# Kernel optimization log

Hardware: AMD Instinct MI355X
Metric: run time of the kernel (lower is better)

The kernel has to match this reference:

```python
import jax, jax.numpy as jnp
import numpy as np

B, K, N, D, H, DOUT = 16, 8, 196, 768, 3072, 768


def setup_inputs() -> dict:
    key = jax.random.key(0)
    ks = jax.random.split(key, 5)
    scale_w1 = 1.0 / np.sqrt(D)
    scale_w2 = 1.0 / np.sqrt(H)
    return {
        "slots": jax.random.normal(ks[0], (B, K, D), dtype=jnp.float32),
        "pos_embed": jax.random.normal(ks[1], (N, D), dtype=jnp.float32) * 0.02,
        "map_alpha": jax.random.normal(ks[2], (N, DOUT), dtype=jnp.float32) * 0.02,
        "W1": jax.random.normal(ks[3], (D, H), dtype=jnp.float32) * scale_w1,
        "b1": jnp.zeros((H,), dtype=jnp.float32),
        "W2": jax.random.normal(ks[4], (H, DOUT), dtype=jnp.float32) * scale_w2,
        "b2": jnp.zeros((DOUT,), dtype=jnp.float32),
    }


def reference(slots, pos_embed, map_alpha, W1, b1, W2, b2):
    b, k, d = slots.shape
    n = pos_embed.shape[0]
    # broadcast slots over patches and add positional embedding: (B,K,N,D)
    tokens = slots[:, :, None, :] + pos_embed[None, None, :, :]
    # 2-layer MLP with ReLU
    h = jax.nn.relu(jnp.einsum('bknd,dh->bknh', tokens, W1) + b1)
    y_k = jnp.einsum('bknh,ho->bkno', h, W2) + b2  # (B,K,N,DOUT)
    # softmax over K of map_alpha expanded over (B,K); identical across K -> uniform 1/K,
    # computed explicitly for faithfulness to the original module
    m_k = jax.nn.softmax(jnp.broadcast_to(map_alpha[None, None, :, :], (b, k, n, map_alpha.shape[1])), axis=1)
    y = jnp.einsum('bknd,bknd->bnd', y_k, m_k)
    return y
```

## Files before the change

### kernel.cpp

```cpp
#include <hip/hip_runtime.h>
#include <hip/hip_bf16.h>
#include <stdint.h>


typedef __attribute__((ext_vector_type(8))) short bf16x8;
typedef __attribute__((ext_vector_type(4))) float f32x4;

#define AS1 __attribute__((address_space(1)))
#define AS3 __attribute__((address_space(3)))

#define WAIT_VM(N) asm volatile("s_waitcnt vmcnt(" #N ")" ::: "memory")
#define BAR()      asm volatile("s_barrier" ::: "memory")
#define BAR_LDS()  asm volatile("s_waitcnt lgkmcnt(0)\ns_barrier" ::: "memory")

static __device__ __forceinline__ void gld_lds16(const void* g, void* l) {
    __builtin_amdgcn_global_load_lds((const AS1 unsigned int*)g,
                                     (AS3 unsigned int*)l, 16, 0, 0);
}

static __device__ __forceinline__ unsigned short f2bf(float f) {
    union { float f; unsigned int u; } v; v.f = f;
    unsigned int u = v.u;
    return (unsigned short)((u + 0x7fffu + ((u >> 16) & 1u)) >> 16);
}

__global__ void k_prep(const float* __restrict__ W1, unsigned short* __restrict__ W1t,
                       const float* __restrict__ S, const float* __restrict__ P,
                       unsigned short* __restrict__ A1) {
    int idx = blockIdx.x * blockDim.x + threadIdx.x;
    const int C1n = 96 * 3072;
    const int PKn = 96 * 384;
    if (idx < C1n) {
        int r  = idx % 3072;
        int kc = idx / 3072;
        unsigned int po[4];
        #pragma unroll
        for (int j = 0; j < 4; ++j) {
            unsigned short lo = f2bf(W1[(size_t)(kc * 8 + 2 * j) * 3072 + r]);
            unsigned short hi = f2bf(W1[(size_t)(kc * 8 + 2 * j + 1) * 3072 + r]);
            po[j] = (unsigned int)lo | ((unsigned int)hi << 16);
        }
        size_t dst = ((size_t)(r >> 6) * 12 + (kc >> 3)) * 4096
                   + (size_t)((kc & 7) * 64 + (r & 63)) * 8;
        *(uint4*)(W1t + dst) = make_uint4(po[0], po[1], po[2], po[3]);
    } else if (idx < C1n + PKn) {
        int t = idx - C1n;
        int r  = t % 384;
        int kc = t / 384;
        uint4 o = make_uint4(0u, 0u, 0u, 0u);
        if (r < 324) {
            const float* src = (r < 128) ? (S + (size_t)r * 768 + kc * 8)
                                         : (P + (size_t)(r - 128) * 768 + kc * 8);
            float4 a = *(const float4*)(src);
            float4 b = *(const float4*)(src + 4);
            o.x = (unsigned int)f2bf(a.x) | ((unsigned int)f2bf(a.y) << 16);
            o.y = (unsigned int)f2bf(a.z) | ((unsigned int)f2bf(a.w) << 16);
            o.z = (unsigned int)f2bf(b.x) | ((unsigned int)f2bf(b.y) << 16);
            o.w = (unsigned int)f2bf(b.z) | ((unsigned int)f2bf(b.w) << 16);
        }
        size_t dst = ((size_t)(r >> 6) * 12 + (kc >> 3)) * 4096
                   + (size_t)((kc & 7) * 64 + (r & 63)) * 8;
        *(uint4*)(A1 + dst) = o;
    }
}

__global__ void k_hbar_w2t(const float* __restrict__ C1, const float* __restrict__ b1,
                           unsigned short* __restrict__ Hb,
                           const float* __restrict__ W2, unsigned short* __restrict__ W2t) {
    const int bid = blockIdx.x;
    const int tid = threadIdx.x;
    if (bid >= 4800) {
        int idx = (bid - 4800) * 256 + tid;
        int r  = idx % 768;
        int kc = idx / 768;
        unsigned int po[4];
        #pragma unroll
        for (int j = 0; j < 4; ++j) {
            unsigned short lo = f2bf(W2[(size_t)(kc * 8 + 2 * j) * 768 + r]);
            unsigned short hi = f2bf(W2[(size_t)(kc * 8 + 2 * j + 1) * 768 + r]);
            po[j] = (unsigned int)lo | ((unsigned int)hi << 16);
        }
        size_t dst = ((size_t)(r >> 6) * 48 + (kc >> 3)) * 4096
                   + (size_t)((kc & 7) * 64 + (r & 63)) * 8;
        *(uint4*)(W2t + dst) = make_uint4(po[0], po[1], po[2], po[3]);
        return;
    }
    const int bx   = bid % 50;
    const int yq   = bid / 50;
    const int lane = tid & 63;
    const int wv   = tid >> 6;
    const int hc   = yq * 4 + wv;
    const int h0   = hc * 8;
    int bn = bx * 64 + lane;
    if (bn > 3135) bn = 3135;
    const int b = bn / 196;
    const int n = bn - b * 196;
    const float* prow = C1 + (size_t)(128 + n) * 3072 + h0;
    float4 pA = *(const float4*)(prow);
    float4 pB = *(const float4*)(prow + 4);
    float4 bA = *(const float4*)(b1 + h0);
    float4 bB = *(const float4*)(b1 + h0 + 4);
    float pb[8] = { pA.x + bA.x, pA.y + bA.y, pA.z + bA.z, pA.w + bA.w,
                    pB.x + bB.x, pB.y + bB.y, pB.z + bB.z, pB.w + bB.w };
    float acc[8] = {};
    #pragma unroll
    for (int k = 0; k < 8; ++k) {
        const float* srow = C1 + (size_t)(b * 8 + k) * 3072 + h0;
        float4 sA_ = *(const float4*)(srow);
        float4 sB_ = *(const float4*)(srow + 4);
        acc[0] += fmaxf(sA_.x + pb[0], 0.f);
        acc[1] += fmaxf(sA_.y + pb[1], 0.f);
        acc[2] += fmaxf(sA_.z + pb[2], 0.f);
        acc[3] += fmaxf(sA_.w + pb[3], 0.f);
        acc[4] += fmaxf(sB_.x + pb[4], 0.f);
        acc[5] += fmaxf(sB_.y + pb[5], 0.f);
        acc[6] += fmaxf(sB_.z + pb[6], 0.f);
        acc[7] += fmaxf(sB_.w + pb[7], 0.f);
    }
    unsigned int w0 = (unsigned int)f2bf(acc[0] * 0.125f) | ((unsigned int)f2bf(acc[1] * 0.125f) << 16);
    unsigned int w1 = (unsigned int)f2bf(acc[2] * 0.125f) | ((unsigned int)f2bf(acc[3] * 0.125f) << 16);
    unsigned int w2 = (unsigned int)f2bf(acc[4] * 0.125f) | ((unsigned int)f2bf(acc[5] * 0.125f) << 16);
    unsigned int w3 = (unsigned int)f2bf(acc[6] * 0.125f) | ((unsigned int)f2bf(acc[7] * 0.125f) << 16);
    size_t dst = ((size_t)bx * 48 + (hc >> 3)) * 4096
               + (size_t)((hc & 7) * 64 + lane) * 8;
    *(uint4*)(Hb + dst) = make_uint4(w0, w1, w2, w3);
}

__launch_bounds__(256)
__global__ void gemm_tiled(const unsigned short* __restrict__ A,
                           const unsigned short* __restrict__ Bt,
                           float* __restrict__ C,
                           int Mstore, int Nd, int KT) {
    __shared__ unsigned short sm[3 * 8192];

    const int tid  = threadIdx.x;
    const int lane = tid & 63;
    const int wave = tid >> 6;
    const int wm = wave >> 1, wn = wave & 1;
    const int q = lane >> 4, l16 = lane & 15;

    const int id = blockIdx.x;
    const int j  = id >> 3;
    const int nt = (id & 7) * 6 + j % 6;
    const int rt = j / 6;

    const unsigned short* Ab = A  + (size_t)rt * KT * 4096;
    const unsigned short* Bb = Bt + (size_t)nt * KT * 4096;

    f32x4 acc[2][2] = {};
    const int offA = (wm * 32 + l16) * 8;
    const int offB = 4096 + (wn * 32 + l16) * 8;

    auto stage = [&](int i, unsigned short* d) {
        const unsigned short* Ag = Ab + (size_t)i * 4096;
        const unsigned short* Bg = Bb + (size_t)i * 4096;
        gld_lds16(Ag + tid * 8,        d + tid * 8);
        gld_lds16(Ag + 2048 + tid * 8, d + 2048 + tid * 8);
        gld_lds16(Bg + tid * 8,        d + 4096 + tid * 8);
        gld_lds16(Bg + 2048 + tid * 8, d + 6144 + tid * 8);
    };
    auto compute = [&](const unsigned short* buf) {
        #pragma unroll
        for (int ks = 0; ks < 2; ++ks) {
            const int ko = (ks * 4 + q) * 512;
            bf16x8 af0 = *(const bf16x8*)(buf + ko + offA);
            bf16x8 af1 = *(const bf16x8*)(buf + ko + offA + 128);
            bf16x8 bf0 = *(const bf16x8*)(buf + ko + offB);
            bf16x8 bf1 = *(const bf16x8*)(buf + ko + offB + 128);
            acc[0][0] = __builtin_amdgcn_mfma_f32_16x16x32_bf16(af0, bf0, acc[0][0], 0, 0, 0);
            acc[0][1] = __builtin_amdgcn_mfma_f32_16x16x32_bf16(af0, bf1, acc[0][1], 0, 0, 0);
            acc[1][0] = __builtin_amdgcn_mfma_f32_16x16x32_bf16(af1, bf0, acc[1][0], 0, 0, 0);
            acc[1][1] = __builtin_amdgcn_mfma_f32_16x16x32_bf16(af1, bf1, acc[1][1], 0, 0, 0);
        }
    };

    unsigned short* s0 = sm;
    unsigned short* s1 = sm + 8192;
    unsigned short* s2 = sm + 16384;

    stage(0, s0);
    stage(1, s1);
    for (int i = 0; i < KT; i += 3) {
        stage(i + 2, s2); WAIT_VM(8);
        BAR(); compute(s0); BAR_LDS();
        if (i + 3 < KT) { stage(i + 3, s0); WAIT_VM(8); } else { WAIT_VM(4); }
        BAR(); compute(s1); BAR_LDS();
        if (i + 4 < KT) { stage(i + 4, s1); WAIT_VM(8); }
        else if (i + 3 < KT) { WAIT_VM(4); }
        else { WAIT_VM(0); }
        BAR(); compute(s2);
        if (i + 3 < KT) BAR_LDS();
    }

    const int row0 = rt * 64 + wm * 32;
    const int col0 = nt * 64 + wn * 32;
    #pragma unroll
    for (int ii = 0; ii < 2; ++ii) {
        #pragma unroll
        for (int jj = 0; jj < 2; ++jj) {
            int col = col0 + jj * 16 + l16;
            #pragma unroll
            for (int r = 0; r < 4; ++r) {
                int row = row0 + ii * 16 + q * 4 + r;
                if (row < Mstore) C[(size_t)row * Nd + col] = acc[ii][jj][r];
            }
        }
    }
}

__launch_bounds__(512)
__global__ void k_gemm2(const unsigned short* __restrict__ Hb,
                        const unsigned short* __restrict__ W2t,
                        const float* __restrict__ b2, float* __restrict__ out) {
    __shared__ unsigned short sm[3 * 12288];

    const int tid  = threadIdx.x;
    const int lane = tid & 63;
    const int wave = tid >> 6;
    const int wm = wave >> 1, wn = wave & 1;
    const int q = lane >> 4, l16 = lane & 15;

    const int id = blockIdx.x;
    int rt, nt;
    if (id < 288) { rt = (id / 96) * 8 + (id & 7); nt = (id % 96) >> 3; }
    else          { rt = 24; nt = id - 288; }

    const unsigned short* A0b = Hb  + ((size_t)(2 * rt)     * 48) * 4096;
    const unsigned short* A1b = Hb  + ((size_t)(2 * rt + 1) * 48) * 4096;
    const unsigned short* Bb  = W2t + ((size_t)nt * 48) * 4096;

    f32x4 acc[2][2] = {};

    auto stage = [&](int i, unsigned short* d) {
        gld_lds16(A0b + (size_t)i * 4096 + tid * 8, d + tid * 8);
        gld_lds16(A1b + (size_t)i * 4096 + tid * 8, d + 4096 + tid * 8);
        gld_lds16(Bb  + (size_t)i * 4096 + tid * 8, d + 8192 + tid * 8);
    };

    const int r0 = wm * 32 + l16;
    const int aoff0 = (r0 >> 6) * 4096 + (r0 & 63) * 8;
    const int r1 = wm * 32 + 16 + l16;
    const int aoff1 = (r1 >> 6) * 4096 + (r1 & 63) * 8;
    const int boff  = 8192 + (wn * 32 + l16) * 8;

    auto compute = [&](const unsigned short* buf) {
        #pragma unroll
        for (int ks = 0; ks < 2; ++ks) {
            const int ko = (ks * 4 + q) * 512;
            bf16x8 af0 = *(const bf16x8*)(buf + aoff0 + ko);
            bf16x8 af1 = *(const bf16x8*)(buf + aoff1 + ko);
            bf16x8 bf0 = *(const bf16x8*)(buf + boff + ko);
            bf16x8 bf1 = *(const bf16x8*)(buf + boff + ko + 128);
            acc[0][0] = __builtin_amdgcn_mfma_f32_16x16x32_bf16(af0, bf0, acc[0][0], 0, 0, 0);
            acc[0][1] = __builtin_amdgcn_mfma_f32_16x16x32_bf16(af0, bf1, acc[0][1], 0, 0, 0);
            acc[1][0] = __builtin_amdgcn_mfma_f32_16x16x32_bf16(af1, bf0, acc[1][0], 0, 0, 0);
            acc[1][1] = __builtin_amdgcn_mfma_f32_16x16x32_bf16(af1, bf1, acc[1][1], 0, 0, 0);
        }
    };

    unsigned short* s0 = sm;
    unsigned short* s1 = sm + 12288;
    unsigned short* s2 = sm + 24576;

    stage(0, s0);
    stage(1, s1);
    for (int i = 0; i < 48; i += 3) {
        stage(i + 2, s2); WAIT_VM(6);
        BAR(); compute(s0); BAR_LDS();
        if (i + 3 < 48) { stage(i + 3, s0); WAIT_VM(6); } else { WAIT_VM(3); }
        BAR(); compute(s1); BAR_LDS();
        if (i + 4 < 48) { stage(i + 4, s1); WAIT_VM(6); }
        else if (i + 3 < 48) { WAIT_VM(3); }
        else { WAIT_VM(0); }
        BAR(); compute(s2);
        if (i + 3 < 48) BAR_LDS();
    }

    const int row0 = rt * 128 + wm * 32;
    const int col0 = nt * 64 + wn * 32;
    #pragma unroll
    for (int ii = 0; ii < 2; ++ii) {
        #pragma unroll
        for (int jj = 0; jj < 2; ++jj) {
            int col = col0 + jj * 16 + l16;
            float bv = b2[col];
            #pragma unroll
            for (int r = 0; r < 4; ++r) {
                int row = row0 + ii * 16 + q * 4 + r;
                if (row < 3136) out[(size_t)row * 768 + col] = acc[ii][jj][r] + bv;
            }
        }
    }
}

extern "C" void kernel_launch(void* const* d_in, const int* in_sizes, int n_in,
                              void* d_out, int out_size, void* d_ws, size_t ws_size,
                              hipStream_t stream) {
    const float* slots  = (const float*)d_in[0];
    const float* pos    = (const float*)d_in[1];
    const float* W1     = (const float*)d_in[3];
    const float* b1     = (const float*)d_in[4];
    const float* W2     = (const float*)d_in[5];
    const float* b2     = (const float*)d_in[6];
    float* out = (float*)d_out;

    size_t off = 0;
    auto alloc = [&](size_t bytes) {
        void* p = (char*)d_ws + off;
        off += (bytes + 255) & ~(size_t)255;
        return p;
    };
    unsigned short* W1t = (unsigned short*)alloc((size_t)3072 * 768 * 2);
    unsigned short* W2t = (unsigned short*)alloc((size_t)768 * 3072 * 2);
    unsigned short* A1  = (unsigned short*)alloc((size_t)384 * 768 * 2);
    float*          C1  = (float*)alloc((size_t)384 * 3072 * 4);
    unsigned short* Hb  = (unsigned short*)alloc((size_t)50 * 48 * 4096 * 2);

    k_prep<<<1296, 256, 0, stream>>>(W1, W1t, slots, pos, A1);
    gemm_tiled<<<288, 256, 0, stream>>>(A1, W1t, C1, 324, 3072, 12);
    k_hbar_w2t<<<5952, 256, 0, stream>>>(C1, b1, Hb, W2, W2t);
    k_gemm2<<<300, 512, 0, stream>>>(Hb, W2t, b2, out);
}
```

Before: 129.9 us.

## Fuse four kernels into one persistent kernel with software grid barriers

Replaces the four separate launches (prep, GEMM1, hbar/W2 transpose, GEMM2) with a single persistent 384-block kernel whose phases are separated by atomic-counter grid barriers. W2 conversion moves into the first prep phase. GEMM1 is retiled to 64x128 tiles with 512 threads, and both GEMMs switch from triple to double buffering. The aim is to remove launch gaps and tail effects, at the cost of spin-wait barriers, fewer blocks for the GEMM phases, and reliance on all 384 blocks being co-resident. The barrier reset scheme via a MAGIC flag in workspace could be fragile across repeated calls.

```diff
diff --git a/kernel.cpp b/kernel.cpp
--- a/kernel.cpp
+++ b/kernel.cpp
@@ -12,6 +12,9 @@
 #define WAIT_VM(N) asm volatile("s_waitcnt vmcnt(" #N ")" ::: "memory")
 #define BAR()      asm volatile("s_barrier" ::: "memory")
 #define BAR_LDS()  asm volatile("s_waitcnt lgkmcnt(0)\ns_barrier" ::: "memory")
+
+#define NB 384u
+#define MAGIC 0x13572468u
 
 static __device__ __forceinline__ void gld_lds16(const void* g, void* l) {
     __builtin_amdgcn_global_load_lds((const AS1 unsigned int*)g,
@@ -24,270 +27,254 @@
     return (unsigned short)((u + 0x7fffu + ((u >> 16) & 1u)) >> 16);
 }
 
-__global__ void k_prep(const float* __restrict__ W1, unsigned short* __restrict__ W1t,
-                       const float* __restrict__ S, const float* __restrict__ P,
-                       unsigned short* __restrict__ A1) {
-    int idx = blockIdx.x * blockDim.x + threadIdx.x;
-    const int C1n = 96 * 3072;
-    const int PKn = 96 * 384;
-    if (idx < C1n) {
-        int r  = idx % 3072;
-        int kc = idx / 3072;
-        unsigned int po[4];
-        #pragma unroll
-        for (int j = 0; j < 4; ++j) {
-            unsigned short lo = f2bf(W1[(size_t)(kc * 8 + 2 * j) * 3072 + r]);
-            unsigned short hi = f2bf(W1[(size_t)(kc * 8 + 2 * j + 1) * 3072 + r]);
-            po[j] = (unsigned int)lo | ((unsigned int)hi << 16);
-        }
-        size_t dst = ((size_t)(r >> 6) * 12 + (kc >> 3)) * 4096
-                   + (size_t)((kc & 7) * 64 + (r & 63)) * 8;
-        *(uint4*)(W1t + dst) = make_uint4(po[0], po[1], po[2], po[3]);
-    } else if (idx < C1n + PKn) {
-        int t = idx - C1n;
-        int r  = t % 384;
-        int kc = t / 384;
-        uint4 o = make_uint4(0u, 0u, 0u, 0u);
-        if (r < 324) {
-            const float* src = (r < 128) ? (S + (size_t)r * 768 + kc * 8)
-                                         : (P + (size_t)(r - 128) * 768 + kc * 8);
-            float4 a = *(const float4*)(src);
-            float4 b = *(const float4*)(src + 4);
-            o.x = (unsigned int)f2bf(a.x) | ((unsigned int)f2bf(a.y) << 16);
-            o.y = (unsigned int)f2bf(a.z) | ((unsigned int)f2bf(a.w) << 16);
-            o.z = (unsigned int)f2bf(b.x) | ((unsigned int)f2bf(b.y) << 16);
-            o.w = (unsigned int)f2bf(b.z) | ((unsigned int)f2bf(b.w) << 16);
-        }
-        size_t dst = ((size_t)(r >> 6) * 12 + (kc >> 3)) * 4096
-                   + (size_t)((kc & 7) * 64 + (r & 63)) * 8;
-        *(uint4*)(A1 + dst) = o;
-    }
-}
-
-__global__ void k_hbar_w2t(const float* __restrict__ C1, const float* __restrict__ b1,
-                           unsigned short* __restrict__ Hb,
-                           const float* __restrict__ W2, unsigned short* __restrict__ W2t) {
-    const int bid = blockIdx.x;
-    const int tid = threadIdx.x;
-    if (bid >= 4800) {
-        int idx = (bid - 4800) * 256 + tid;
-        int r  = idx % 768;
-        int kc = idx / 768;
-        unsigned int po[4];
-        #pragma unroll
-        for (int j = 0; j < 4; ++j) {
-            unsigned short lo = f2bf(W2[(size_t)(kc * 8 + 2 * j) * 768 + r]);
-            unsigned short hi = f2bf(W2[(size_t)(kc * 8 + 2 * j + 1) * 768 + r]);
-            po[j] = (unsigned int)lo | ((unsigned int)hi << 16);
-        }
-        size_t dst = ((size_t)(r >> 6) * 48 + (kc >> 3)) * 4096
-                   + (size_t)((kc & 7) * 64 + (r & 63)) * 8;
-        *(uint4*)(W2t + dst) = make_uint4(po[0], po[1], po[2], po[3]);
-        return;
-    }
-    const int bx   = bid % 50;
-    const int yq   = bid / 50;
-    const int lane = tid & 63;
-    const int wv   = tid >> 6;
-    const int hc   = yq * 4 + wv;
-    const int h0   = hc * 8;
-    int bn = bx * 64 + lane;
-    if (bn > 3135) bn = 3135;
-    const int b = bn / 196;
-    const int n = bn - b * 196;
-    const float* prow = C1 + (size_t)(128 + n) * 3072 + h0;
-    float4 pA = *(const float4*)(prow);
-    float4 pB = *(const float4*)(prow + 4);
-    float4 bA = *(const float4*)(b1 + h0);
-    float4 bB = *(const float4*)(b1 + h0 + 4);
-    float pb[8] = { pA.x + bA.x, pA.y + bA.y, pA.z + bA.z, pA.w + bA.w,
-                    pB.x + bB.x, pB.y + bB.y, pB.z + bB.z, pB.w + bB.w };
-    float acc[8] = {};
-    #pragma unroll
-    for (int k = 0; k < 8; ++k) {
-        const float* srow = C1 + (size_t)(b * 8 + k) * 3072 + h0;
-        float4 sA_ = *(const float4*)(srow);
-        float4 sB_ = *(const float4*)(srow + 4);
-        acc[0] += fmaxf(sA_.x + pb[0], 0.f);
-        acc[1] += fmaxf(sA_.y + pb[1], 0.f);
-        acc[2] += fmaxf(sA_.z + pb[2], 0.f);
-        acc[3] += fmaxf(sA_.w + pb[3], 0.f);
-        acc[4] += fmaxf(sB_.x + pb[4], 0.f);
-        acc[5] += fmaxf(sB_.y + pb[5], 0.f);
-        acc[6] += fmaxf(sB_.z + pb[6], 0.f);
-        acc[7] += fmaxf(sB_.w + pb[7], 0.f);
-    }
-    unsigned int w0 = (unsigned int)f2bf(acc[0] * 0.125f) | ((unsigned int)f2bf(acc[1] * 0.125f) << 16);
-    unsigned int w1 = (unsigned int)f2bf(acc[2] * 0.125f) | ((unsigned int)f2bf(acc[3] * 0.125f) << 16);
-    unsigned int w2 = (unsigned int)f2bf(acc[4] * 0.125f) | ((unsigned int)f2bf(acc[5] * 0.125f) << 16);
-    unsigned int w3 = (unsigned int)f2bf(acc[6] * 0.125f) | ((unsigned int)f2bf(acc[7] * 0.125f) << 16);
-    size_t dst = ((size_t)bx * 48 + (hc >> 3)) * 4096
-               + (size_t)((hc & 7) * 64 + lane) * 8;
-    *(uint4*)(Hb + dst) = make_uint4(w0, w1, w2, w3);
-}
-
-__launch_bounds__(256)
-__global__ void gemm_tiled(const unsigned short* __restrict__ A,
-                           const unsigned short* __restrict__ Bt,
-                           float* __restrict__ C,
-                           int Mstore, int Nd, int KT) {
-    __shared__ unsigned short sm[3 * 8192];
-
+static __device__ __forceinline__ void grid_barrier(unsigned* slot) {
+    __syncthreads();
+    if (threadIdx.x == 0) {
+        __threadfence();
+        __hip_atomic_fetch_add(slot, 1u, __ATOMIC_ACQ_REL, __HIP_MEMORY_SCOPE_AGENT);
+        while (__hip_atomic_load(slot, __ATOMIC_RELAXED, __HIP_MEMORY_SCOPE_AGENT) < NB)
+            __builtin_amdgcn_s_sleep(16);
+        __threadfence();
+    }
+    __syncthreads();
+}
+
+__launch_bounds__(512, 4)
+__global__ void k_fused(const float* __restrict__ slots, const float* __restrict__ pos,
+                        const float* __restrict__ W1, const float* __restrict__ b1,
+                        const float* __restrict__ W2, const float* __restrict__ b2,
+                        unsigned* __restrict__ bar,
+                        unsigned short* __restrict__ W1t, unsigned short* __restrict__ W2t,
+                        unsigned short* __restrict__ A1, float* __restrict__ C1,
+                        unsigned short* __restrict__ Hb, float* __restrict__ out) {
+    __shared__ unsigned short sm[2 * 12288];
     const int tid  = threadIdx.x;
     const int lane = tid & 63;
     const int wave = tid >> 6;
-    const int wm = wave >> 1, wn = wave & 1;
-    const int q = lane >> 4, l16 = lane & 15;
-
-    const int id = blockIdx.x;
-    const int j  = id >> 3;
-    const int nt = (id & 7) * 6 + j % 6;
-    const int rt = j / 6;
-
-    const unsigned short* Ab = A  + (size_t)rt * KT * 4096;
-    const unsigned short* Bb = Bt + (size_t)nt * KT * 4096;
-
-    f32x4 acc[2][2] = {};
-    const int offA = (wm * 32 + l16) * 8;
-    const int offB = 4096 + (wn * 32 + l16) * 8;
-
-    auto stage = [&](int i, unsigned short* d) {
-        const unsigned short* Ag = Ab + (size_t)i * 4096;
-        const unsigned short* Bg = Bb + (size_t)i * 4096;
-        gld_lds16(Ag + tid * 8,        d + tid * 8);
-        gld_lds16(Ag + 2048 + tid * 8, d + 2048 + tid * 8);
-        gld_lds16(Bg + tid * 8,        d + 4096 + tid * 8);
-        gld_lds16(Bg + 2048 + tid * 8, d + 6144 + tid * 8);
-    };
-    auto compute = [&](const unsigned short* buf) {
+    const int q    = lane >> 4;
+    const int l16  = lane & 15;
+
+    if (blockIdx.x == 0 && tid == 0) {
+        __hip_atomic_store(&bar[1], 0u, __ATOMIC_RELAXED, __HIP_MEMORY_SCOPE_AGENT);
+        __hip_atomic_store(&bar[2], 0u, __ATOMIC_RELAXED, __HIP_MEMORY_SCOPE_AGENT);
+        __hip_atomic_store(&bar[3], 0u, __ATOMIC_RELAXED, __HIP_MEMORY_SCOPE_AGENT);
+        __hip_atomic_store(&bar[0], MAGIC, __ATOMIC_RELEASE, __HIP_MEMORY_SCOPE_AGENT);
+    }
+
+    for (int idx = blockIdx.x * 512 + tid; idx < 626688; idx += NB * 512) {
+        if (idx < 294912) {
+            int r  = idx % 3072;
+            int kc = idx / 3072;
+            unsigned int po[4];
+            #pragma unroll
+            for (int j = 0; j < 4; ++j) {
+                unsigned short lo = f2bf(W1[(size_t)(kc * 8 + 2 * j) * 3072 + r]);
+                unsigned short hi = f2bf(W1[(size_t)(kc * 8 + 2 * j + 1) * 3072 + r]);
+                po[j] = (unsigned int)lo | ((unsigned int)hi << 16);
+            }
+            size_t dst = ((size_t)(r >> 6) * 12 + (kc >> 3)) * 4096
+                       + (size_t)((kc & 7) * 64 + (r & 63)) * 8;
+            *(uint4*)(W1t + dst) = make_uint4(po[0], po[1], po[2], po[3]);
+        } else if (idx < 331776) {
+            int t = idx - 294912;
+            int r  = t % 384;
+            int kc = t / 384;
+            uint4 o = make_uint4(0u, 0u, 0u, 0u);
+            if (r < 324) {
+                const float* src = (r < 128) ? (slots + (size_t)r * 768 + kc * 8)
+                                             : (pos + (size_t)(r - 128) * 768 + kc * 8);
+                float4 a = *(const float4*)(src);
+                float4 b = *(const float4*)(src + 4);
+                o.x = (unsigned int)f2bf(a.x) | ((unsigned int)f2bf(a.y) << 16);
+                o.y = (unsigned int)f2bf(a.z) | ((unsigned int)f2bf(a.w) << 16);
+                o.z = (unsigned int)f2bf(b.x) | ((unsigned int)f2bf(b.y) << 16);
+                o.w = (unsigned int)f2bf(b.z) | ((unsigned int)f2bf(b.w) << 16);
+            }
+            size_t dst = ((size_t)(r >> 6) * 12 + (kc >> 3)) * 4096
+                       + (size_t)((kc & 7) * 64 + (r & 63)) * 8;
+            *(uint4*)(A1 + dst) = o;
+        } else {
+            int t = idx - 331776;
+            int r  = t % 768;
+            int kc = t / 768;
+            unsigned int po[4];
+            #pragma unroll
+            for (int j = 0; j < 4; ++j) {
+                unsigned short lo = f2bf(W2[(size_t)(kc * 8 + 2 * j) * 768 + r]);
+                unsigned short hi = f2bf(W2[(size_t)(kc * 8 + 2 * j + 1) * 768 + r]);
+                po[j] = (unsigned int)lo | ((unsigned int)hi << 16);
+            }
+            size_t dst = ((size_t)(r >> 6) * 48 + (kc >> 3)) * 4096
+                       + (size_t)((kc & 7) * 64 + (r & 63)) * 8;
+            *(uint4*)(W2t + dst) = make_uint4(po[0], po[1], po[2], po[3]);
+        }
+    }
+    __syncthreads();
+    if (tid == 0) {
+        while (__hip_atomic_load(&bar[0], __ATOMIC_RELAXED, __HIP_MEMORY_SCOPE_AGENT) != MAGIC)
+            __builtin_amdgcn_s_sleep(16);
+        __threadfence();
+        __hip_atomic_fetch_add(&bar[1], 1u, __ATOMIC_ACQ_REL, __HIP_MEMORY_SCOPE_AGENT);
+        while (__hip_atomic_load(&bar[1], __ATOMIC_RELAXED, __HIP_MEMORY_SCOPE_AGENT) < NB)
+            __builtin_amdgcn_s_sleep(16);
+        __threadfence();
+    }
+    __syncthreads();
+
+    if (blockIdx.x < 144) {
+        const int rt = blockIdx.x / 24;
+        const int nt = blockIdx.x % 24;
+        const unsigned short* Ab = A1  + (size_t)rt * 12 * 4096;
+        const unsigned short* B0 = W1t + (size_t)(2 * nt)     * 12 * 4096;
+        const unsigned short* B1 = W1t + (size_t)(2 * nt + 1) * 12 * 4096;
+        const int wm = wave >> 2;
+        const int wn = wave & 3;
+        f32x4 acc[2][2] = {};
+        auto stage = [&](int i, unsigned short* d) {
+            gld_lds16(Ab + (size_t)i * 4096 + tid * 8, d + tid * 8);
+            gld_lds16(B0 + (size_t)i * 4096 + tid * 8, d + 4096 + tid * 8);
+            gld_lds16(B1 + (size_t)i * 4096 + tid * 8, d + 8192 + tid * 8);
+        };
+        const int aoff = (wm * 32 + l16) * 8;
+        const int boff = 4096 + (wn >> 1) * 4096 + ((wn & 1) * 32 + l16) * 8;
+        auto compute = [&](const unsigned short* buf) {
+            #pragma unroll
+            for (int ks = 0; ks < 2; ++ks) {
+                const int ko = (ks * 4 + q) * 512;
+                bf16x8 af0 = *(const bf16x8*)(buf + ko + aoff);
+                bf16x8 af1 = *(const bf16x8*)(buf + ko + aoff + 128);
+                bf16x8 bf0 = *(const bf16x8*)(buf + ko + boff);
+                bf16x8 bf1 = *(const bf16x8*)(buf + ko + boff + 128);
+                acc[0][0] = __builtin_amdgcn_mfma_f32_16x16x32_bf16(af0, bf0, acc[0][0], 0, 0, 0);
+                acc[0][1] = __builtin_amdgcn_mfma_f32_16x16x32_bf16(af0, bf1, acc[0][1], 0, 0, 0);
+                acc[1][0] = __builtin_amdgcn_mfma_f32_16x16x32_bf16(af1, bf0, acc[1][0], 0, 0, 0);
+                acc[1][1] = __builtin_amdgcn_mfma_f32_16x16x32_bf16(af1, bf1, acc[1][1], 0, 0, 0);
+            }
+        };
+        stage(0, sm);
+        #pragma unroll 1
+        for (int i = 0; i < 12; ++i) {
+            unsigned short* cur = sm + (i & 1) * 12288;
+            unsigned short* nxt = sm + ((i + 1) & 1) * 12288;
+            if (i + 1 < 12) { stage(i + 1, nxt); WAIT_VM(3); } else { WAIT_VM(0); }
+            BAR();
+            compute(cur);
+            if (i + 1 < 12) BAR_LDS();
+        }
+        const int row0 = rt * 64 + wm * 32;
+        const int col0 = nt * 128 + ((wn >> 1) * 64) + (wn & 1) * 32;
         #pragma unroll
-        for (int ks = 0; ks < 2; ++ks) {
-            const int ko = (ks * 4 + q) * 512;
-            bf16x8 af0 = *(const bf16x8*)(buf + ko + offA);
-            bf16x8 af1 = *(const bf16x8*)(buf + ko + offA + 128);
-            bf16x8 bf0 = *(const bf16x8*)(buf + ko + offB);
-            bf16x8 bf1 = *(const bf16x8*)(buf + ko + offB + 128);
-            acc[0][0] = __builtin_amdgcn_mfma_f32_16x16x32_bf16(af0, bf0, acc[0][0], 0, 0, 0);
-            acc[0][1] = __builtin_amdgcn_mfma_f32_16x16x32_bf16(af0, bf1, acc[0][1], 0, 0, 0);
-            acc[1][0] = __builtin_amdgcn_mfma_f32_16x16x32_bf16(af1, bf0, acc[1][0], 0, 0, 0);
-            acc[1][1] = __builtin_amdgcn_mfma_f32_16x16x32_bf16(af1, bf1, acc[1][1], 0, 0, 0);
-        }
-    };
-
-    unsigned short* s0 = sm;
-    unsigned short* s1 = sm + 8192;
-    unsigned short* s2 = sm + 16384;
-
-    stage(0, s0);
-    stage(1, s1);
-    for (int i = 0; i < KT; i += 3) {
-        stage(i + 2, s2); WAIT_VM(8);
-        BAR(); compute(s0); BAR_LDS();
-        if (i + 3 < KT) { stage(i + 3, s0); WAIT_VM(8); } else { WAIT_VM(4); }
-        BAR(); compute(s1); BAR_LDS();
-        if (i + 4 < KT) { stage(i + 4, s1); WAIT_VM(8); }
-        else if (i + 3 < KT) { WAIT_VM(4); }
-        else { WAIT_VM(0); }
-        BAR(); compute(s2);
-        if (i + 3 < KT) BAR_LDS();
-    }
-
-    const int row0 = rt * 64 + wm * 32;
-    const int col0 = nt * 64 + wn * 32;
-    #pragma unroll
-    for (int ii = 0; ii < 2; ++ii) {
+        for (int ii = 0; ii < 2; ++ii) {
+            #pragma unroll
+            for (int jj = 0; jj < 2; ++jj) {
+                int col = col0 + jj * 16 + l16;
+                #pragma unroll
+                for (int r = 0; r < 4; ++r) {
+                    int row = row0 + ii * 16 + q * 4 + r;
+                    if (row < 324) C1[(size_t)row * 3072 + col] = acc[ii][jj][r];
+                }
+            }
+        }
+    }
+    grid_barrier(&bar[2]);
+
+    for (int u = blockIdx.x; u < 2400; u += NB) {
+        const int bx = u / 48;
+        const int hg = u - bx * 48;
+        const int hc = hg * 8 + wave;
+        const int h0 = hc * 8;
+        int bn = bx * 64 + lane;
+        if (bn > 3135) bn = 3135;
+        const int b = bn / 196;
+        const int n = bn - b * 196;
+        const float* prow = C1 + (size_t)(128 + n) * 3072 + h0;
+        float4 pA = *(const float4*)(prow);
+        float4 pB = *(const float4*)(prow + 4);
+        float4 bA = *(const float4*)(b1 + h0);
+        float4 bB = *(const float4*)(b1 + h0 + 4);
+        float pb[8] = { pA.x + bA.x, pA.y + bA.y, pA.z + bA.z, pA.w + bA.w,
+                        pB.x + bB.x, pB.y + bB.y, pB.z + bB.z, pB.w + bB.w };
+        float acc[8] = {};
         #pragma unroll
-        for (int jj = 0; jj < 2; ++jj) {
-            int col = col0 + jj * 16 + l16;
-            #pragma unroll
-            for (int r = 0; r < 4; ++r) {
-                int row = row0 + ii * 16 + q * 4 + r;
-                if (row < Mstore) C[(size_t)row * Nd + col] = acc[ii][jj][r];
-            }
-        }
-    }
-}
-
-__launch_bounds__(512)
-__global__ void k_gemm2(const unsigned short* __restrict__ Hb,
-                        const unsigned short* __restrict__ W2t,
-                        const float* __restrict__ b2, float* __restrict__ out) {
-    __shared__ unsigned short sm[3 * 12288];
-
-    const int tid  = threadIdx.x;
-    const int lane = tid & 63;
-    const int wave = tid >> 6;
-    const int wm = wave >> 1, wn = wave & 1;
-    const int q = lane >> 4, l16 = lane & 15;
-
-    const int id = blockIdx.x;
-    int rt, nt;
-    if (id < 288) { rt = (id / 96) * 8 + (id & 7); nt = (id % 96) >> 3; }
-    else          { rt = 24; nt = id - 288; }
-
-    const unsigned short* A0b = Hb  + ((size_t)(2 * rt)     * 48) * 4096;
-    const unsigned short* A1b = Hb  + ((size_t)(2 * rt + 1) * 48) * 4096;
-    const unsigned short* Bb  = W2t + ((size_t)nt * 48) * 4096;
-
-    f32x4 acc[2][2] = {};
-
-    auto stage = [&](int i, unsigned short* d) {
-        gld_lds16(A0b + (size_t)i * 4096 + tid * 8, d + tid * 8);
-        gld_lds16(A1b + (size_t)i * 4096 + tid * 8, d + 4096 + tid * 8);
-        gld_lds16(Bb  + (size_t)i * 4096 + tid * 8, d + 8192 + tid * 8);
-    };
-
-    const int r0 = wm * 32 + l16;
-    const int aoff0 = (r0 >> 6) * 4096 + (r0 & 63) * 8;
-    const int r1 = wm * 32 + 16 + l16;
-    const int aoff1 = (r1 >> 6) * 4096 + (r1 & 63) * 8;
-    const int boff  = 8192 + (wn * 32 + l16) * 8;
-
-    auto compute = [&](const unsigned short* buf) {
+        for (int k = 0; k < 8; ++k) {
+            const float* srow = C1 + (size_t)(b * 8 + k) * 3072 + h0;
+            float4 sA_ = *(const float4*)(srow);
+            float4 sB_ = *(const float4*)(srow + 4);
+            acc[0] += fmaxf(sA_.x + pb[0], 0.f);
+            acc[1] += fmaxf(sA_.y + pb[1], 0.f);
+            acc[2] += fmaxf(sA_.z + pb[2], 0.f);
+            acc[3] += fmaxf(sA_.w + pb[3], 0.f);
+            acc[4] += fmaxf(sB_.x + pb[4], 0.f);
+            acc[5] += fmaxf(sB_.y + pb[5], 0.f);
+            acc[6] += fmaxf(sB_.z + pb[6], 0.f);
+            acc[7] += fmaxf(sB_.w + pb[7], 0.f);
+        }
+        unsigned int w0 = (unsigned int)f2bf(acc[0] * 0.125f) | ((unsigned int)f2bf(acc[1] * 0.125f) << 16);
+        unsigned int w1 = (unsigned int)f2bf(acc[2] * 0.125f) | ((unsigned int)f2bf(acc[3] * 0.125f) << 16);
+        unsigned int w2 = (unsigned int)f2bf(acc[4] * 0.125f) | ((unsigned int)f2bf(acc[5] * 0.125f) << 16);
+        unsigned int w3 = (unsigned int)f2bf(acc[6] * 0.125f) | ((unsigned int)f2bf(acc[7] * 0.125f) << 16);
+        size_t dst = ((size_t)bx * 48 + hg) * 4096 + (size_t)(wave * 64 + lane) * 8;
+        *(uint4*)(Hb + dst) = make_uint4(w0, w1, w2, w3);
+    }
+    grid_barrier(&bar[3]);
+
+    if (blockIdx.x < 300) {
+        const int id = blockIdx.x;
+        int rt, nt;
+        if (id < 288) { rt = (id / 96) * 8 + (id & 7); nt = (id % 96) >> 3; }
+        else          { rt = 24; nt = id - 288; }
+        const unsigned short* A0b = Hb  + ((size_t)(2 * rt)     * 48) * 4096;
+        const unsigned short* A1b = Hb  + ((size_t)(2 * rt + 1) * 48) * 4096;
+        const unsigned short* Bb  = W2t + ((size_t)nt * 48) * 4096;
+        const int wm = wave >> 1, wn = wave & 1;
+        f32x4 acc[2][2] = {};
+        auto stage = [&](int i, unsigned short* d) {
+            gld_lds16(A0b + (size_t)i * 4096 + tid * 8, d + tid * 8);
+            gld_lds16(A1b + (size_t)i * 4096 + tid * 8, d + 4096 + tid * 8);
+            gld_lds16(Bb  + (size_t)i * 4096 + tid * 8, d + 8192 + tid * 8);
+        };
+        const int r0 = wm * 32 + l16;
+        const int aoff0 = (r0 >> 6) * 4096 + (r0 & 63) * 8;
+        const int r1 = wm * 32 + 16 + l16;
+        const int aoff1 = (r1 >> 6) * 4096 + (r1 & 63) * 8;
+        const int boff  = 8192 + (wn * 32 + l16) * 8;
+        auto compute = [&](const unsigned short* buf) {
+            #pragma unroll
+            for (int ks = 0; ks < 2; ++ks) {
+                const int ko = (ks * 4 + q) * 512;
+                bf16x8 af0 = *(const bf16x8*)(buf + aoff0 + ko);
+                bf16x8 af1 = *(const bf16x8*)(buf + aoff1 + ko);
+                bf16x8 bf0 = *(const bf16x8*)(buf + boff + ko);
+                bf16x8 bf1 = *(const bf16x8*)(buf + boff + ko + 128);
+                acc[0][0] = __builtin_amdgcn_mfma_f32_16x16x32_bf16(af0, bf0, acc[0][0], 0, 0, 0);
+                acc[0][1] = __builtin_amdgcn_mfma_f32_16x16x32_bf16(af0, bf1, acc[0][1], 0, 0, 0);
+                acc[1][0] = __builtin_amdgcn_mfma_f32_16x16x32_bf16(af1, bf0, acc[1][0], 0, 0, 0);
+                acc[1][1] = __builtin_amdgcn_mfma_f32_16x16x32_bf16(af1, bf1, acc[1][1], 0, 0, 0);
+            }
+        };
+        stage(0, sm);
+        #pragma unroll 1
+        for (int i = 0; i < 48; ++i) {
+            unsigned short* cur = sm + (i & 1) * 12288;
+            unsigned short* nxt = sm + ((i + 1) & 1) * 12288;
+            if (i + 1 < 48) { stage(i + 1, nxt); WAIT_VM(3); } else { WAIT_VM(0); }
+            BAR();
+            compute(cur);
+            if (i + 1 < 48) BAR_LDS();
+        }
+        const int row0 = rt * 128 + wm * 32;
+        const int col0 = nt * 64 + wn * 32;
         #pragma unroll
-        for (int ks = 0; ks < 2; ++ks) {
-            const int ko = (ks * 4 + q) * 512;
-            bf16x8 af0 = *(const bf16x8*)(buf + aoff0 + ko);
-            bf16x8 af1 = *(const bf16x8*)(buf + aoff1 + ko);
-            bf16x8 bf0 = *(const bf16x8*)(buf + boff + ko);
-            bf16x8 bf1 = *(const bf16x8*)(buf + boff + ko + 128);
-            acc[0][0] = __builtin_amdgcn_mfma_f32_16x16x32_bf16(af0, bf0, acc[0][0], 0, 0, 0);
-            acc[0][1] = __builtin_amdgcn_mfma_f32_16x16x32_bf16(af0, bf1, acc[0][1], 0, 0, 0);
-            acc[1][0] = __builtin_amdgcn_mfma_f32_16x16x32_bf16(af1, bf0, acc[1][0], 0, 0, 0);
-            acc[1][1] = __builtin_amdgcn_mfma_f32_16x16x32_bf16(af1, bf1, acc[1][1], 0, 0, 0);
-        }
-    };
-
-    unsigned short* s0 = sm;
-    unsigned short* s1 = sm + 12288;
-    unsigned short* s2 = sm + 24576;
-
-    stage(0, s0);
-    stage(1, s1);
-    for (int i = 0; i < 48; i += 3) {
-        stage(i + 2, s2); WAIT_VM(6);
-        BAR(); compute(s0); BAR_LDS();
-        if (i + 3 < 48) { stage(i + 3, s0); WAIT_VM(6); } else { WAIT_VM(3); }
-        BAR(); compute(s1); BAR_LDS();
-        if (i + 4 < 48) { stage(i + 4, s1); WAIT_VM(6); }
-        else if (i + 3 < 48) { WAIT_VM(3); }
-        else { WAIT_VM(0); }
-        BAR(); compute(s2);
-        if (i + 3 < 48) BAR_LDS();
-    }
-
-    const int row0 = rt * 128 + wm * 32;
-    const int col0 = nt * 64 + wn * 32;
-    #pragma unroll
-    for (int ii = 0; ii < 2; ++ii) {
-        #pragma unroll
-        for (int jj = 0; jj < 2; ++jj) {
-            int col = col0 + jj * 16 + l16;
-            float bv = b2[col];
-            #pragma unroll
-            for (int r = 0; r < 4; ++r) {
-                int row = row0 + ii * 16 + q * 4 + r;
-                if (row < 3136) out[(size_t)row * 768 + col] = acc[ii][jj][r] + bv;
+        for (int ii = 0; ii < 2; ++ii) {
+            #pragma unroll
+            for (int jj = 0; jj < 2; ++jj) {
+                int col = col0 + jj * 16 + l16;
+                float bv = b2[col];
+                #pragma unroll
+                for (int r = 0; r < 4; ++r) {
+                    int row = row0 + ii * 16 + q * 4 + r;
+                    if (row < 3136) out[(size_t)row * 768 + col] = acc[ii][jj][r] + bv;
+                }
             }
         }
     }
@@ -310,14 +297,13 @@
         off += (bytes + 255) & ~(size_t)255;
         return p;
     };
+    unsigned*       bar = (unsigned*)alloc(256);
     unsigned short* W1t = (unsigned short*)alloc((size_t)3072 * 768 * 2);
     unsigned short* W2t = (unsigned short*)alloc((size_t)768 * 3072 * 2);
     unsigned short* A1  = (unsigned short*)alloc((size_t)384 * 768 * 2);
     float*          C1  = (float*)alloc((size_t)384 * 3072 * 4);
     unsigned short* Hb  = (unsigned short*)alloc((size_t)50 * 48 * 4096 * 2);
 
-    k_prep<<<1296, 256, 0, stream>>>(W1, W1t, slots, pos, A1);
-    gemm_tiled<<<288, 256, 0, stream>>>(A1, W1t, C1, 324, 3072, 12);
-    k_hbar_w2t<<<5952, 256, 0, stream>>>(C1, b1, Hb, W2, W2t);
-    k_gemm2<<<300, 512, 0, stream>>>(Hb, W2t, b2, out);
-}
+    k_fused<<<384, 512, 0, stream>>>(slots, pos, W1, b1, W2, b2,
+                                     bar, W1t, W2t, A1, C1, Hb, out);
+}
```

Result: slower. 286.1 us (+120.3%).
